# Kernel optimization log

Measured on AMD Instinct MI355X. Metric: run time of the kernel, lower is better.

Reference implementation:

```python
import jax, jax.numpy as jnp
from jax import lax
import numpy as np

HID = 150     # FFNN hidden dim
EMB = 300     # GloVe dim (input_dim)
LSTM = 200    # lstm_dim -> state_dim = 400
T = 768       # tokens in doc
VOCAB = 50000


def _ffnn(x, W1, b1, W2, b2, W3, b3):
    h = jax.nn.relu(x @ W1.T + b1)
    h = jax.nn.relu(h @ W2.T + b2)
    return h @ W3.T + b3


def _lstm_dir(x, Wih, Whh, b):
    H = Whh.shape[1]
    def step(carry, xt):
        h, c = carry
        z = xt @ Wih.T + h @ Whh.T + b
        i, f, g, o = jnp.split(z, 4, axis=-1)
        c = jax.nn.sigmoid(f) * c + jax.nn.sigmoid(i) * jnp.tanh(g)
        h = jax.nn.sigmoid(o) * jnp.tanh(c)
        return (h, c), h
    init = (jnp.zeros((H,), x.dtype), jnp.zeros((H,), x.dtype))
    _, hs = lax.scan(step, init, x)
    return hs


def setup_inputs():
    key = jax.random.key(0)
    ks = iter(jax.random.split(key, 40))
    def w(shape, s=0.05):
        return jax.random.normal(next(ks), shape, jnp.float32) * s
    state = 2 * LSTM
    span = 2 * state + EMB + 1   # 1101
    pair = 3 * span              # 3303
    z = lambda n: jnp.zeros((n,), jnp.float32)
    return {
        'tokens': jax.random.randint(next(ks), (T,), 0, VOCAB),
        'emb': w((VOCAB, EMB), 0.3),
        'Wih_f': w((4 * LSTM, EMB)), 'Whh_f': w((4 * LSTM, LSTM)), 'b_f': z(4 * LSTM),
        'Wih_b': w((4 * LSTM, EMB)), 'Whh_b': w((4 * LSTM, LSTM)), 'b_b': z(4 * LSTM),
        'aW1': w((HID, state)), 'ab1': z(HID), 'aW2': w((HID, HID)), 'ab2': z(HID), 'aW3': w((1, HID)), 'ab3': z(1),
        'sW1': w((HID, span)), 'sb1': z(HID), 'sW2': w((HID, HID)), 'sb2': z(HID), 'sW3': w((1, HID)), 'sb3': z(1),
        'pW1': w((HID, pair)), 'pb1': z(HID), 'pW2': w((HID, HID)), 'pb2': z(HID), 'pW3': w((1, HID)), 'pb3': z(1),
    }


def reference(tokens, emb, Wih_f, Whh_f, b_f, Wih_b, Whh_b, b_b,
              aW1, ab1, aW2, ab2, aW3, ab3,
              sW1, sb1, sW2, sb2, sW3, sb3,
              pW1, pb1, pW2, pb2, pW3, pb3):
    Tn = tokens.shape[0]
    x = emb[tokens]  # (T, 300) frozen GloVe embeds
    h = jnp.concatenate([_lstm_dir(x, Wih_f, Whh_f, b_f),
                         _lstm_dir(x[::-1], Wih_b, Whh_b, b_b)[::-1]], axis=-1)  # (T, 400)
    # dropout omitted (eval mode / identity)
    attn_logits = _ffnn(h, aW1, ab1, aW2, ab2, aW3, ab3)[:, 0]  # per-token attn score (T,)
    gs, i1s, i2s = [], [], []
    for n in range(1, 11):  # span widths 1..10
        starts = jnp.arange(Tn - n + 1)
        idx = starts[:, None] + jnp.arange(n)[None, :]           # (S_n, n)
        wgt = jax.nn.softmax(attn_logits[idx], axis=-1)          # per-span softmax over LSTM-state scores
        pooled = jnp.einsum('sn,snd->sd', wgt, x[idx])           # attention pools raw embeds (as original)
        g = jnp.concatenate([h[starts], h[starts + n - 1], pooled,
                             jnp.full((Tn - n + 1, 1), float(n), jnp.float32)], axis=-1)
        gs.append(g); i1s.append(starts); i2s.append(starts + n - 1)
    g = jnp.concatenate(gs, 0)                                    # (S, 1101)
    i1 = jnp.concatenate(i1s, 0); i2 = jnp.concatenate(i2s, 0)
    S = g.shape[0]
    sm = _ffnn(g, sW1, sb1, sW2, sb2, sW3, sb3)[:, 0]             # span scores (S,)
    order = jnp.argsort(-sm)                                      # stable desc sort, as Python sorted(reverse=True)
    i1o, i2o = i1[order], i2[order]
    # greedy overlap filter: keep span if fully taken OR both endpoints free; mark taken only when kept
    def body(k, carry):
        taken, keep = carry
        a, b = i1o[k], i2o[k]
        offs = jnp.clip(a + jnp.arange(10), 0, Tn - 1)
        valid = (a + jnp.arange(10)) <= b
        all_taken = jnp.all(jnp.where(valid, taken[offs], True))
        ok = all_taken | (~taken[a] & ~taken[b])
        keep = keep.at[k].set(ok)
        taken = taken.at[offs].max(valid & ok)
        return (taken, keep)
    _, keep = lax.fori_loop(0, S, body, (jnp.zeros((Tn,), bool), jnp.zeros((S,), bool)))
    K = int(round(Tn * 0.4))
    rank = jnp.cumsum(keep.astype(jnp.int32))
    pos = jnp.where(keep & (rank <= K), rank - 1, S)
    sel = jnp.argsort(pos)[:K]            # first K kept spans, score order (>=T width-1 spans always kept)
    sel = sel[jnp.argsort(i1o[sel])]      # stable sort by span start
    g_f = g[order][sel]; sm_f = sm[order][sel]
    i1_f = i1o[sel]; i2_f = i2o[sel]
    ii, jj = np.tril_indices(K, -1)       # row-major == nested (i, j<i) loop order
    pairs = jnp.concatenate([g_f[ii], g_f[jj], g_f[ii] * g_f[jj]], axis=-1)  # (P, 3303)
    sa = _ffnn(pairs, pW1, pb1, pW2, pb2, pW3, pb3)[:, 0]
    # sij[i, j] = sm_i + sm_j + sa_ij for j < i; diag/upper = 0 (the epsilon antecedent)
    sij = jnp.zeros((K, K), jnp.float32).at[ii, jj].set(sm_f[ii] + sm_f[jj] + sa)
    return sij, i1_f, i2_f
```

## Files before the change

kernel.cpp:

```cpp
#include <hip/hip_runtime.h>
#include <hip/hip_bf16.h>
#include <math.h>
#include <float.h>

#define TN      768
#define EMBD    300
#define XPAD    304
#define LSTMD   200
#define G4      800
#define STATE   400
#define HIDD    150
#define NPADC   160
#define SPAND   1101
#define KP      1120
#define NSPANS  7635
#define NSEL    307
#define SORTN   8192

typedef unsigned long long ull;
typedef __attribute__((ext_vector_type(8))) short bf16x8;
typedef __attribute__((ext_vector_type(4))) float mf32x4;

#define OFF_X       0u
#define OFF_ZXF     233472u
#define OFF_ZXB     847872u
#define OFF_H       1462272u
#define OFF_ATTN    1769472u
#define OFF_I1      1770496u
#define OFF_I2      1778176u
#define OFF_SM      1785856u
#define OFF_SELK    1793536u
#define OFF_SELSPAN 1794048u
#define OFF_SMF     1794560u
#define OFF_A       1795072u
#define OFF_B       1844224u
#define OFF_WTF     1893376u
#define OFF_WTB     2133376u
#define OFF_AW1T    2373376u
#define OFF_AW2T    2437376u
#define OFF_SW1T    2461376u
#define OFF_SW2T    2640576u
#define OFF_PW1AT   2664576u
#define OFF_PW1BT   2843776u
#define OFF_PW1CT   3022976u
#define OFF_PW2T    3202176u
#define OFF_G       3226176u
#define OFF_PW1CB   11777376u
#define OFF_PW2B    11866976u

#define REP50(M) M(0) M(1) M(2) M(3) M(4) M(5) M(6) M(7) M(8) M(9) \
 M(10) M(11) M(12) M(13) M(14) M(15) M(16) M(17) M(18) M(19) \
 M(20) M(21) M(22) M(23) M(24) M(25) M(26) M(27) M(28) M(29) \
 M(30) M(31) M(32) M(33) M(34) M(35) M(36) M(37) M(38) M(39) \
 M(40) M(41) M(42) M(43) M(44) M(45) M(46) M(47) M(48) M(49)

__device__ __forceinline__ float sigf(float x) { return 1.f / (1.f + __expf(-x)); }
__device__ __forceinline__ float tanhf_(float x) {
    x = fminf(15.f, fmaxf(-15.f, x));
    float e = __expf(2.f * x);
    return (e - 1.f) / (e + 1.f);
}
__device__ __forceinline__ unsigned short f2bf(float v) {
    __hip_bfloat16 h = __float2bfloat16(v);
    return *(unsigned short*)&h;
}

__global__ void k_gather(const int* __restrict__ tokens, const float* __restrict__ emb,
                         float* __restrict__ x) {
    int t = blockIdx.x;
    int tok = tokens[t];
    for (int d = threadIdx.x; d < XPAD; d += 256)
        x[t * XPAD + d] = (d < EMBD) ? emb[(size_t)tok * EMBD + d] : 0.f;
}

__global__ void k_transpose(const float* __restrict__ src, float* __restrict__ dst,
                            int N, int K, int srcStride, int colOff, int Npad) {
    int k = blockIdx.x;
    int n = blockIdx.y * 256 + threadIdx.x;
    if (n >= Npad) return;
    float v = 0.f;
    if (k < K && n < N) v = src[(size_t)n * srcStride + colOff + k];
    dst[(size_t)k * Npad + n] = v;
}

__global__ void k_bf16w(const float* __restrict__ pW1, const float* __restrict__ pW2,
                        unsigned short* __restrict__ pw1cb,
                        unsigned short* __restrict__ pw2b) {
    int r = blockIdx.x;
    for (int k = threadIdx.x; k < 1120; k += 256) {
        float v = (r < 150 && k < 1101) ? pW1[(size_t)r * 3303 + 2202 + k] : 0.f;
        pw1cb[(size_t)r * 1120 + k] = f2bf(v);
    }
    for (int k = threadIdx.x; k < 160; k += 256) {
        float v = (r < 150 && k < 150) ? pW2[(size_t)r * 150 + k] : 0.f;
        pw2b[(size_t)r * 160 + k] = f2bf(v);
    }
}

__global__ void k_zx(const float* __restrict__ x, const float* __restrict__ WTf,
                     const float* __restrict__ WTb, const float* __restrict__ bf,
                     const float* __restrict__ bb, float* __restrict__ zxf,
                     float* __restrict__ zxb) {
    __shared__ float xl[8 * XPAD];
    int tid = threadIdx.x;
    int bm = blockIdx.x, dir = blockIdx.y;
    for (int l = tid; l < 8 * XPAD; l += 256) xl[l] = x[(size_t)(bm * 8) * XPAD + l];
    __syncthreads();
    const float* WT = dir ? WTb : WTf;
    const float* bv = dir ? bb : bf;
    float* zx = dir ? zxb : zxf;
    for (int jj = 0; jj < 4; ++jj) {
        int n = tid + 256 * jj;
        if (n >= G4) break;
        float acc[8] = {0, 0, 0, 0, 0, 0, 0, 0};
        for (int k = 0; k < EMBD; ++k) {
            float wv = WT[(size_t)k * G4 + n];
#pragma unroll
            for (int r = 0; r < 8; ++r) acc[r] = fmaf(xl[r * XPAD + k], wv, acc[r]);
        }
        float bias = bv[n];
#pragma unroll
        for (int r = 0; r < 8; ++r) {
            int row = bm * 8 + r;
            int trow = dir ? (TN - 1 - row) : row;
            zx[(size_t)trow * G4 + n] = acc[r] + bias;
        }
    }
}

__global__ __launch_bounds__(256, 1) void k_lstm_mb8(const float* __restrict__ zxf,
                                                     const float* __restrict__ zxb,
                                                     const float* __restrict__ Whh_f,
                                                     const float* __restrict__ Whh_b,
                                                     float* __restrict__ hcat,
                                                     ull* __restrict__ hqL2,
                                                     ull* __restrict__ hqL3) {
    int blk = blockIdx.x;
    int lane8 = blk & 7;
    if (lane8 >= 2) return;
    int dir = lane8, b = blk >> 3;
    int tid = threadIdx.x;

    const float* zx = dir ? zxb : zxf;
    const float* Whh = dir ? Whh_b : Whh_f;
    ull* hq2d = hqL2 + (size_t)dir * TN * 256;
    ull* hq3d = hqL3 + (size_t)dir * TN * 256;
    __shared__ __align__(16) float hprev[LSTMD];
    __shared__ float zl[200];
    bool active = tid < 200;
    int q = tid / 50, u = tid % 50;
    int gr_row = q * 200 + b * 50 + u;
    int grs = active ? gr_row : 0;
    const float4* wr = (const float4*)(Whh + (size_t)grs * LSTMD);
#define WDECL(i) float4 w##i = wr[i];
    REP50(WDECL)
#undef WDECL
    float c = 0.f;
    for (int l = tid; l < LSTMD; l += 256) hprev[l] = 0.f;
    int remote_idx = (tid < b * 50) ? tid : tid + 50;
    int use_fast = 4;
    __syncthreads();
    float zpre = zx[grs];
    for (int t = 0; t < TN; ++t) {
        float acc = zpre;
        const float4* h4 = (const float4*)hprev;
#define WFMA(i) { float4 hv = h4[i]; \
        acc = fmaf(w##i.x, hv.x, acc); acc = fmaf(w##i.y, hv.y, acc); \
        acc = fmaf(w##i.z, hv.z, acc); acc = fmaf(w##i.w, hv.w, acc); }
        REP50(WFMA)
#undef WFMA
        if (active) zl[tid] = acc;
        __syncthreads();
        int trow = dir ? (TN - 1 - t) : t;
        if (tid < 50) {
            float zi = zl[tid], zf = zl[50 + tid], zg = zl[100 + tid], zo = zl[150 + tid];
            c = sigf(zf) * c + sigf(zi) * tanhf_(zg);
            float h = sigf(zo) * tanhf_(c);
            hcat[(size_t)trow * STATE + dir * LSTMD + b * 50 + tid] = h;
            hprev[b * 50 + tid] = h;
            if (t + 1 < TN) {
                ull pk = (ull)__float_as_uint(h) | ((ull)(unsigned)(t + 1) << 32);
                size_t slot = (size_t)t * 256 + b * 50 + tid;
                (void)__hip_atomic_exchange(&hq2d[slot], pk, __ATOMIC_RELAXED,
                                            __HIP_MEMORY_SCOPE_WORKGROUP);
                __hip_atomic_store(&hq3d[slot], pk, __ATOMIC_RELAXED,
                                   __HIP_MEMORY_SCOPE_AGENT);
            }
        }
        if (t + 1 < TN) {
            zpre = zx[(size_t)(t + 1) * G4 + grs];
            if (tid < 150) {
                size_t slot = (size_t)t * 256 + remote_idx;
                ull v = 0;
                bool got = false;
                if (use_fast > 0) {
                    for (int it = 0; it < 8; ++it) {
                        ull probe = ~0ull;
                        __hip_atomic_compare_exchange_strong(
                            &hq2d[slot], &probe, ~0ull, __ATOMIC_RELAXED,
                            __ATOMIC_RELAXED, __HIP_MEMORY_SCOPE_WORKGROUP);
                        if ((unsigned)(probe >> 32) == (unsigned)(t + 1)) {
                            v = probe; got = true; break;
                        }
                    }
                    use_fast = got ? 4 : (use_fast - 1);
                }
                if (!got) {
                    do {
                        v = __hip_atomic_load(&hq3d[slot], __ATOMIC_RELAXED,
                                              __HIP_MEMORY_SCOPE_AGENT);
                    } while ((unsigned)(v >> 32) != (unsigned)(t + 1));
                }
                hprev[remote_idx] = __uint_as_float((unsigned)v);
            }
            __syncthreads();
        }
    }
}

__global__ void k_attn(const float* __restrict__ hcat, const float* __restrict__ aW1T,
                       const float* __restrict__ ab1, const float* __restrict__ aW2T,
                       const float* __restrict__ ab2, const float* __restrict__ aW3,
                       const float* __restrict__ ab3, float* __restrict__ attn) {
    __shared__ float hrow[STATE];
    __shared__ float l1[NPADC];
    __shared__ float l2[NPADC];
    __shared__ float red[256];
    int t = blockIdx.x, tid = threadIdx.x;
    for (int d = tid; d < STATE; d += 256) hrow[d] = hcat[(size_t)t * STATE + d];
    __syncthreads();
    if (tid < HIDD) {
        float acc = ab1[tid];
        for (int k = 0; k < STATE; ++k) acc = fmaf(hrow[k], aW1T[(size_t)k * NPADC + tid], acc);
        l1[tid] = fmaxf(acc, 0.f);
    }
    __syncthreads();
    if (tid < HIDD) {
        float acc = ab2[tid];
        for (int k = 0; k < HIDD; ++k) acc = fmaf(l1[k], aW2T[(size_t)k * NPADC + tid], acc);
        l2[tid] = fmaxf(acc, 0.f);
    }
    __syncthreads();
    float partial = (tid < HIDD) ? l2[tid] * aW3[tid] : 0.f;
    red[tid] = partial;
    __syncthreads();
    for (int s = 128; s > 0; s >>= 1) {
        if (tid < s) red[tid] += red[tid + s];
        __syncthreads();
    }
    if (tid == 0) attn[t] = red[0] + ab3[0];
}

__global__ void k_spans(const float* __restrict__ attn, const float* __restrict__ hcat,
                        const float* __restrict__ x, float* __restrict__ g,
                        int* __restrict__ i1s, int* __restrict__ i2s) {
    int s = blockIdx.x;
    int n = 1, base = 0;
    while (s >= base + (TN - n + 1)) { base += TN - n + 1; n++; }
    int a = s - base, b = a + n - 1;
    int lane = threadIdx.x;
    float e[10];
    float mx = -FLT_MAX;
#pragma unroll
    for (int k = 0; k < 10; ++k)
        if (k < n) { e[k] = attn[a + k]; mx = fmaxf(mx, e[k]); }
    float ssum = 0.f;
#pragma unroll
    for (int k = 0; k < 10; ++k)
        if (k < n) { e[k] = __expf(e[k] - mx); ssum += e[k]; }
    float w[10];
#pragma unroll
    for (int k = 0; k < 10; ++k) w[k] = (k < n) ? e[k] / ssum : 0.f;

    float* grow = g + (size_t)s * KP;
    for (int d = lane; d < STATE; d += 64) grow[d] = hcat[(size_t)a * STATE + d];
    for (int d = lane; d < STATE; d += 64) grow[STATE + d] = hcat[(size_t)b * STATE + d];
    for (int d = lane; d < EMBD; d += 64) {
        float p = 0.f;
#pragma unroll
        for (int k = 0; k < 10; ++k)
            if (k < n) p = fmaf(w[k], x[(size_t)(a + k) * XPAD + d], p);
        grow[2 * STATE + d] = p;
    }
    if (lane == 0) { grow[1100] = (float)n; i1s[s] = a; i2s[s] = b; }
    for (int d = SPAND + lane; d < KP; d += 64) grow[d] = 0.f;
}

__global__ void k_sm(const float* __restrict__ g, const float* __restrict__ sW1T,
                     const float* __restrict__ sb1, const float* __restrict__ sW2T,
                     const float* __restrict__ sb2, const float* __restrict__ sW3,
                     const float* __restrict__ sb3, float* __restrict__ smo) {
    __shared__ float As[32 * 33];
    __shared__ float Bs[32 * NPADC];
    __shared__ float L1[32 * 161];
    int tid = threadIdx.x;
    int tx = tid & 31, ty = tid >> 5;
    int row0 = blockIdx.x * 32;
    float acc[4][5] = {};
    for (int kb = 0; kb < KP; kb += 32) {
        for (int l = tid; l < 32 * 32; l += 256) {
            int r = l >> 5, cc = l & 31;
            int gr = row0 + r;
            As[r * 33 + cc] = (gr < NSPANS) ? g[(size_t)gr * KP + kb + cc] : 0.f;
        }
        for (int l = tid; l < 32 * NPADC; l += 256) {
            int r = l / NPADC, cc = l - NPADC * r;
            Bs[l] = sW1T[(size_t)(kb + r) * NPADC + cc];
        }
        __syncthreads();
        for (int kk = 0; kk < 32; ++kk) {
            float bv[5];
#pragma unroll
            for (int jn = 0; jn < 5; ++jn) bv[jn] = Bs[kk * NPADC + tx + 32 * jn];
#pragma unroll
            for (int i4 = 0; i4 < 4; ++i4) {
                float av = As[(ty * 4 + i4) * 33 + kk];
#pragma unroll
                for (int jn = 0; jn < 5; ++jn) acc[i4][jn] = fmaf(av, bv[jn], acc[i4][jn]);
            }
        }
        __syncthreads();
    }
#pragma unroll
    for (int i4 = 0; i4 < 4; ++i4)
#pragma unroll
        for (int jn = 0; jn < 5; ++jn) {
            int nn = tx + 32 * jn;
            float v = acc[i4][jn] + (nn < HIDD ? sb1[nn] : 0.f);
            L1[(ty * 4 + i4) * 161 + nn] = fmaxf(v, 0.f);
        }
    __syncthreads();
    float acc2[4][5] = {};
    for (int kk = 0; kk < HIDD; ++kk) {
        float bv[5];
#pragma unroll
        for (int jn = 0; jn < 5; ++jn) bv[jn] = sW2T[(size_t)kk * NPADC + tx + 32 * jn];
#pragma unroll
        for (int i4 = 0; i4 < 4; ++i4) {
            float av = L1[(ty * 4 + i4) * 161 + kk];
#pragma unroll
            for (int jn = 0; jn < 5; ++jn) acc2[i4][jn] = fmaf(av, bv[jn], acc2[i4][jn]);
        }
    }
    float part[4];
#pragma unroll
    for (int i4 = 0; i4 < 4; ++i4) {
        float p = 0.f;
#pragma unroll
        for (int jn = 0; jn < 5; ++jn) {
            int nn = tx + 32 * jn;
            float v = acc2[i4][jn] + (nn < HIDD ? sb2[nn] : 0.f);
            v = fmaxf(v, 0.f);
            p = fmaf(v, (nn < HIDD ? sW3[nn] : 0.f), p);
        }
        part[i4] = p;
    }
    for (int s = 16; s > 0; s >>= 1)
#pragma unroll
        for (int i4 = 0; i4 < 4; ++i4) part[i4] += __shfl_xor(part[i4], s, 32);
    if (tx == 0)
#pragma unroll
        for (int i4 = 0; i4 < 4; ++i4) {
            int gr = row0 + ty * 4 + i4;
            if (gr < NSPANS) smo[gr] = part[i4] + sb3[0];
        }
}

__global__ __launch_bounds__(1024) void k_sortsel(const float* __restrict__ sm,
                                                  const int* __restrict__ i1s,
                                                  const int* __restrict__ i2s,
                                                  int* __restrict__ selk,
                                                  int* __restrict__ selspan,
                                                  float* __restrict__ smf,
                                                  float* __restrict__ out) {
    __shared__ float ks[SORTN];
    __shared__ unsigned short id16[SORTN];
    __shared__ int ka2[512];
    __shared__ int va2[512];
    int tid = threadIdx.x;
    for (int i = tid; i < SORTN; i += 1024) {
        ks[i] = (i < NSPANS) ? sm[i] : -FLT_MAX;
        id16[i] = (unsigned short)i;
    }
    __syncthreads();
    for (int size = 2; size <= SORTN; size <<= 1) {
        for (int stride = size >> 1; stride > 0; stride >>= 1) {
            for (int t = tid; t < SORTN / 2; t += 1024) {
                int i = ((t & ~(stride - 1)) << 1) | (t & (stride - 1));
                int j = i + stride;
                float ki = ks[i], kj = ks[j];
                unsigned short ai = id16[i], aj = id16[j];
                bool less_ji = (kj > ki) || (kj == ki && aj < ai);
                bool asc = ((i & size) == 0);
                if (less_ji == asc) {
                    ks[i] = kj; ks[j] = ki;
                    id16[i] = aj; id16[j] = ai;
                }
            }
            __syncthreads();
        }
    }
    unsigned* abu = reinterpret_cast<unsigned*>(ks);
    for (int k = tid; k < NSPANS; k += 1024) {
        int sid = id16[k];
        abu[k] = (unsigned)i1s[sid] | ((unsigned)i2s[sid] << 16);
    }
    __syncthreads();
    if (tid < 64) {
        int l = tid;
        unsigned tk = 0;
        int cnt = 0;
        for (int k = 0; k < NSPANS && cnt < NSEL; ++k) {
            unsigned ab = abu[k];
            int a = (int)(ab & 0xFFFFu), b = (int)(ab >> 16);
            int lo = a - (l << 5), hi = b - (l << 5);
            lo = lo < 0 ? 0 : lo;
            hi = hi > 31 ? 31 : hi;
            unsigned m = 0;
            if (hi >= lo) {
                unsigned upper = (hi == 31) ? 0xFFFFFFFFu : ((1u << (hi + 1)) - 1u);
                m = upper & ~((1u << lo) - 1u);
            }
            bool cov = ((tk & m) == m);
            bool all_taken = __all((int)cov);
            int la = a >> 5, lb = b >> 5;
            unsigned long long bal_a = __ballot((int)((l == la) && ((tk >> (a & 31)) & 1u)));
            unsigned long long bal_b = __ballot((int)((l == lb) && ((tk >> (b & 31)) & 1u)));
            bool ok = all_taken || (bal_a == 0ull && bal_b == 0ull);
            if (ok) {
                tk |= m;
                if (l == 0) selk[cnt] = k;
                cnt++;
            }
        }
    }
    __syncthreads();
    if (tid < 512) {
        int r = tid;
        int key = 0x7FFFFFFF;
        if (r < NSEL) {
            int k = selk[r];
            int a = (int)(abu[k] & 0xFFFFu);
            key = (a << 9) | r;
        }
        ka2[r] = key;
        va2[r] = r;
    }
    __syncthreads();
    for (int size = 2; size <= 512; size <<= 1) {
        for (int stride = size >> 1; stride > 0; stride >>= 1) {
            if (tid < 256) {
                int t = tid;
                int i = ((t & ~(stride - 1)) << 1) | (t & (stride - 1));
                int j = i + stride;
                int ki = ka2[i], kj = ka2[j];
                bool asc = ((i & size) == 0);
                if ((kj < ki) == asc) {
                    ka2[i] = kj; ka2[j] = ki;
                    int vi = va2[i]; va2[i] = va2[j]; va2[j] = vi;
                }
            }
            __syncthreads();
        }
    }
    if (tid < NSEL) {
        int r = va2[tid];
        int k = selk[r];
        int sid = id16[k];
        unsigned ab = abu[k];
        selspan[tid] = sid;
        smf[tid] = sm[sid];
        out[NSEL * NSEL + tid] = (float)(ab & 0xFFFFu);
        out[NSEL * NSEL + NSEL + tid] = (float)(ab >> 16);
    }
}

__global__ void k_AB(const float* __restrict__ g, const int* __restrict__ selspan,
                     const float* __restrict__ pW1aT, const float* __restrict__ pW1bT,
                     const float* __restrict__ pb1, float* __restrict__ Aw,
                     float* __restrict__ Bw) {
    __shared__ float grow[KP];
    int r = blockIdx.x, which = blockIdx.y;
    int sid = selspan[r];
    int tid = threadIdx.x;
    for (int d = tid; d < KP; d += 256) grow[d] = g[(size_t)sid * KP + d];
    __syncthreads();
    if (tid < NPADC) {
        const float* WT = which ? pW1bT : pW1aT;
        float acc = 0.f;
        for (int k = 0; k < KP; ++k) acc = fmaf(grow[k], WT[(size_t)k * NPADC + tid], acc);
        if (which == 0) acc += (tid < HIDD ? pb1[tid] : 0.f);
        (which ? Bw : Aw)[(size_t)r * NPADC + tid] = acc;
    }
}

__global__ __launch_bounds__(256, 1) void k_pairs_mfma(
    const float* __restrict__ g, const int* __restrict__ selspan,
    const float* __restrict__ smf, const float* __restrict__ Aw,
    const float* __restrict__ Bw, const unsigned short* __restrict__ pw1cb,
    const unsigned short* __restrict__ pw2b, const float* __restrict__ pb2,
    const float* __restrict__ pW3, const float* __restrict__ pb3,
    float* __restrict__ out) {
    int i = blockIdx.x;
    int j0 = blockIdx.y * 32;
    if (j0 >= i) return;
    __shared__ __align__(16) unsigned short Abuf[32][232];
    __shared__ __align__(16) unsigned short Btb[160][232];
    __shared__ __align__(16) unsigned short L1b[32][168];
    __shared__ float BwS[32][160];
    __shared__ float AwS[160];
    __shared__ float GiS[224];
    __shared__ float pb2S[160], pw3S[160];
    __shared__ float parts[4][32];
    int tid = threadIdx.x;
    int lane = tid & 63, wv = tid >> 6;
    int l15 = lane & 15, lg = lane >> 4;
    int sidi = selspan[i];

    if (tid < 160) {
        AwS[tid] = Aw[(size_t)i * NPADC + tid];
        pb2S[tid] = (tid < HIDD) ? pb2[tid] : 0.f;
        pw3S[tid] = (tid < HIDD) ? pW3[tid] : 0.f;
    }
    for (int idx = tid; idx < 32 * 160; idx += 256) {
        int r = idx / 160; int c = idx - r * 160;
        int j = j0 + r;
        BwS[r][c] = Bw[(size_t)(j < i ? j : 0) * NPADC + c];
    }
    mf32x4 acc[2][3];
#pragma unroll
    for (int m = 0; m < 2; ++m)
#pragma unroll
        for (int t = 0; t < 3; ++t) acc[m][t] = (mf32x4){0.f, 0.f, 0.f, 0.f};

    for (int kc = 0; kc < KP; kc += 224) {
        if (tid < 56)
            *(float4*)&GiS[tid * 4] = *(const float4*)&g[(size_t)sidi * KP + kc + tid * 4];
        for (int idx = tid; idx < 160 * 28; idx += 256) {
            int r = idx / 28, s = idx - r * 28;
            uint4 v = *(const uint4*)(pw1cb + (size_t)r * 1120 + kc + s * 8);
            *(uint4*)&Btb[r][s * 8] = v;
        }
        __syncthreads();
        for (int idx = tid; idx < 32 * 56; idx += 256) {
            int r = idx / 56, s = idx - r * 56;
            int j = j0 + r;
            float4 gj = {0.f, 0.f, 0.f, 0.f};
            if (j < i) gj = *(const float4*)&g[(size_t)selspan[j] * KP + kc + s * 4];
            float4 gi = *(const float4*)&GiS[s * 4];
            ushort4 u;
            u.x = f2bf(gj.x * gi.x); u.y = f2bf(gj.y * gi.y);
            u.z = f2bf(gj.z * gi.z); u.w = f2bf(gj.w * gi.w);
            *(ushort4*)&Abuf[r][s * 4] = u;
        }
        __syncthreads();
#pragma unroll
        for (int kk = 0; kk < 7; ++kk) {
            int ko = kk * 32 + lg * 8;
            bf16x8 a0 = *(const bf16x8*)&Abuf[l15][ko];
            bf16x8 a1 = *(const bf16x8*)&Abuf[16 + l15][ko];
#pragma unroll
            for (int t = 0; t < 3; ++t) {
                int n = wv + 4 * t;
                if (n < 10) {
                    bf16x8 bb = *(const bf16x8*)&Btb[n * 16 + l15][ko];
                    acc[0][t] = __builtin_amdgcn_mfma_f32_16x16x32_bf16(a0, bb, acc[0][t], 0, 0, 0);
                    acc[1][t] = __builtin_amdgcn_mfma_f32_16x16x32_bf16(a1, bb, acc[1][t], 0, 0, 0);
                }
            }
        }
        __syncthreads();
    }
#pragma unroll
    for (int m = 0; m < 2; ++m)
#pragma unroll
        for (int t = 0; t < 3; ++t) {
            int n = wv + 4 * t;
            if (n < 10) {
#pragma unroll
                for (int q = 0; q < 4; ++q) {
                    int row = m * 16 + lg * 4 + q;
                    int col = n * 16 + l15;
                    float v = acc[m][t][q] + AwS[col] + BwS[row][col];
                    L1b[row][col] = f2bf(fmaxf(v, 0.f));
                }
            }
        }
    for (int idx = tid; idx < 160 * 20; idx += 256) {
        int r = idx / 20, s = idx - r * 20;
        *(uint4*)&Btb[r][s * 8] = *(const uint4*)(pw2b + (size_t)r * 160 + s * 8);
    }
    __syncthreads();
    mf32x4 acc2[2][3];
#pragma unroll
    for (int m = 0; m < 2; ++m)
#pragma unroll
        for (int t = 0; t < 3; ++t) acc2[m][t] = (mf32x4){0.f, 0.f, 0.f, 0.f};
#pragma unroll
    for (int kk = 0; kk < 5; ++kk) {
        int ko = kk * 32 + lg * 8;
        bf16x8 a0 = *(const bf16x8*)&L1b[l15][ko];
        bf16x8 a1 = *(const bf16x8*)&L1b[16 + l15][ko];
#pragma unroll
        for (int t = 0; t < 3; ++t) {
            int n = wv + 4 * t;
            if (n < 10) {
                bf16x8 bb = *(const bf16x8*)&Btb[n * 16 + l15][ko];
                acc2[0][t] = __builtin_amdgcn_mfma_f32_16x16x32_bf16(a0, bb, acc2[0][t], 0, 0, 0);
                acc2[1][t] = __builtin_amdgcn_mfma_f32_16x16x32_bf16(a1, bb, acc2[1][t], 0, 0, 0);
            }
        }
    }
    float s[2][4] = {};
#pragma unroll
    for (int m = 0; m < 2; ++m)
#pragma unroll
        for (int t = 0; t < 3; ++t) {
            int n = wv + 4 * t;
            if (n < 10) {
#pragma unroll
                for (int q = 0; q < 4; ++q) {
                    int col = n * 16 + l15;
                    float v = fmaxf(acc2[m][t][q] + pb2S[col], 0.f);
                    s[m][q] = fmaf(v, pw3S[col], s[m][q]);
                }
            }
        }
#pragma unroll
    for (int off = 1; off < 16; off <<= 1)
#pragma unroll
        for (int m = 0; m < 2; ++m)
#pragma unroll
            for (int q = 0; q < 4; ++q) s[m][q] += __shfl_xor(s[m][q], off);
    if (l15 == 0) {
#pragma unroll
        for (int m = 0; m < 2; ++m)
#pragma unroll
            for (int q = 0; q < 4; ++q) parts[wv][m * 16 + lg * 4 + q] = s[m][q];
    }
    __syncthreads();
    if (tid < 32) {
        float sa = parts[0][tid] + parts[1][tid] + parts[2][tid] + parts[3][tid];
        int j = j0 + tid;
        if (j < i) out[(size_t)i * NSEL + j] = smf[i] + smf[j] + sa + pb3[0];
    }
}

extern "C" void kernel_launch(void* const* d_in, const int* in_sizes, int n_in,
                              void* d_out, int out_size, void* d_ws, size_t ws_size,
                              hipStream_t stream) {
    (void)in_sizes; (void)n_in; (void)ws_size;
    const int* tokens  = (const int*)d_in[0];
    const float* emb   = (const float*)d_in[1];
    const float* Wih_f = (const float*)d_in[2];
    const float* Whh_f = (const float*)d_in[3];
    const float* b_f   = (const float*)d_in[4];
    const float* Wih_b = (const float*)d_in[5];
    const float* Whh_b = (const float*)d_in[6];
    const float* b_b   = (const float*)d_in[7];
    const float* aW1 = (const float*)d_in[8];  const float* ab1 = (const float*)d_in[9];
    const float* aW2 = (const float*)d_in[10]; const float* ab2 = (const float*)d_in[11];
    const float* aW3 = (const float*)d_in[12]; const float* ab3 = (const float*)d_in[13];
    const float* sW1 = (const float*)d_in[14]; const float* sb1 = (const float*)d_in[15];
    const float* sW2 = (const float*)d_in[16]; const float* sb2 = (const float*)d_in[17];
    const float* sW3 = (const float*)d_in[18]; const float* sb3 = (const float*)d_in[19];
    const float* pW1 = (const float*)d_in[20]; const float* pb1 = (const float*)d_in[21];
    const float* pW2 = (const float*)d_in[22]; const float* pb2 = (const float*)d_in[23];
    const float* pW3 = (const float*)d_in[24]; const float* pb3 = (const float*)d_in[25];
    float* W = (float*)d_ws;
    float* out = (float*)d_out;
    ull* hqL2 = (ull*)(W + OFF_G);
    ull* hqL3 = hqL2 + (size_t)2 * TN * 256;
    unsigned short* pw1cb = (unsigned short*)(W + OFF_PW1CB);
    unsigned short* pw2b  = (unsigned short*)(W + OFF_PW2B);

    hipMemsetAsync(d_out, 0, (size_t)out_size * sizeof(float), stream);
    hipMemsetAsync(hqL2, 0, (size_t)4 * TN * 256 * sizeof(ull), stream);

    k_gather<<<TN, 256, 0, stream>>>(tokens, emb, W + OFF_X);

    k_transpose<<<dim3(300, 4), 256, 0, stream>>>(Wih_f, W + OFF_WTF, 800, 300, 300, 0, 800);
    k_transpose<<<dim3(300, 4), 256, 0, stream>>>(Wih_b, W + OFF_WTB, 800, 300, 300, 0, 800);
    k_transpose<<<dim3(400, 1), 256, 0, stream>>>(aW1, W + OFF_AW1T, 150, 400, 400, 0, NPADC);
    k_transpose<<<dim3(150, 1), 256, 0, stream>>>(aW2, W + OFF_AW2T, 150, 150, 150, 0, NPADC);
    k_transpose<<<dim3(KP, 1), 256, 0, stream>>>(sW1, W + OFF_SW1T, 150, SPAND, SPAND, 0, NPADC);
    k_transpose<<<dim3(150, 1), 256, 0, stream>>>(sW2, W + OFF_SW2T, 150, 150, 150, 0, NPADC);
    k_transpose<<<dim3(KP, 1), 256, 0, stream>>>(pW1, W + OFF_PW1AT, 150, SPAND, 3303, 0, NPADC);
    k_transpose<<<dim3(KP, 1), 256, 0, stream>>>(pW1, W + OFF_PW1BT, 150, SPAND, 3303, 1101, NPADC);
    k_bf16w<<<160, 256, 0, stream>>>(pW1, pW2, pw1cb, pw2b);

    k_zx<<<dim3(96, 2), 256, 0, stream>>>(W + OFF_X, W + OFF_WTF, W + OFF_WTB, b_f, b_b,
                                          W + OFF_ZXF, W + OFF_ZXB);
    k_lstm_mb8<<<32, 256, 0, stream>>>(W + OFF_ZXF, W + OFF_ZXB, Whh_f, Whh_b, W + OFF_H,
                                       hqL2, hqL3);
    k_attn<<<TN, 256, 0, stream>>>(W + OFF_H, W + OFF_AW1T, ab1, W + OFF_AW2T, ab2, aW3, ab3,
                                   W + OFF_ATTN);
    k_spans<<<NSPANS, 64, 0, stream>>>(W + OFF_ATTN, W + OFF_H, W + OFF_X, W + OFF_G,
                                       (int*)(W + OFF_I1), (int*)(W + OFF_I2));
    k_sm<<<(NSPANS + 31) / 32, 256, 0, stream>>>(W + OFF_G, W + OFF_SW1T, sb1, W + OFF_SW2T, sb2,
                                                 sW3, sb3, W + OFF_SM);
    k_sortsel<<<1, 1024, 0, stream>>>(W + OFF_SM, (int*)(W + OFF_I1), (int*)(W + OFF_I2),
                                      (int*)(W + OFF_SELK), (int*)(W + OFF_SELSPAN),
                                      W + OFF_SMF, out);
    k_AB<<<dim3(NSEL, 2), 256, 0, stream>>>(W + OFF_G, (int*)(W + OFF_SELSPAN), W + OFF_PW1AT,
                                            W + OFF_PW1BT, pb1, W + OFF_A, W + OFF_B);
    k_pairs_mfma<<<dim3(NSEL, 10), 256, 0, stream>>>(W + OFF_G, (int*)(W + OFF_SELSPAN),
                                                     W + OFF_SMF, W + OFF_A, W + OFF_B,
                                                     pw1cb, pw2b, pb2, pW3, pb3, out);
}
```

Before: 2.218 ms.

## Fold weight prep into LSTM kernel blocks and merge gather/transpose launches

Merges the embedding gather and both Wih transposes into one launch. The remaining weight transposes and bf16 conversions move into extra blocks of the LSTM kernel, so they run alongside the serial recurrence instead of as separate launches. The LSTM dot product is also split across four accumulators to shorten the dependent FMA chain. This cuts kernel launch count and hides prep work behind the latency-bound LSTM, at the risk of the extra blocks competing with LSTM blocks for CUs or memory bandwidth. The four-way split also changes the floating-point summation order slightly.

```diff
diff --git a/kernel.cpp b/kernel.cpp
--- a/kernel.cpp
+++ b/kernel.cpp
@@ -42,8 +42,6 @@
 #define OFF_SW2T    2640576u
 #define OFF_PW1AT   2664576u
 #define OFF_PW1BT   2843776u
-#define OFF_PW1CT   3022976u
-#define OFF_PW2T    3202176u
 #define OFF_G       3226176u
 #define OFF_PW1CB   11777376u
 #define OFF_PW2B    11866976u
@@ -65,35 +63,23 @@
     return *(unsigned short*)&h;
 }
 
-__global__ void k_gather(const int* __restrict__ tokens, const float* __restrict__ emb,
-                         float* __restrict__ x) {
-    int t = blockIdx.x;
-    int tok = tokens[t];
-    for (int d = threadIdx.x; d < XPAD; d += 256)
-        x[t * XPAD + d] = (d < EMBD) ? emb[(size_t)tok * EMBD + d] : 0.f;
-}
-
-__global__ void k_transpose(const float* __restrict__ src, float* __restrict__ dst,
-                            int N, int K, int srcStride, int colOff, int Npad) {
-    int k = blockIdx.x;
-    int n = blockIdx.y * 256 + threadIdx.x;
-    if (n >= Npad) return;
-    float v = 0.f;
-    if (k < K && n < N) v = src[(size_t)n * srcStride + colOff + k];
-    dst[(size_t)k * Npad + n] = v;
-}
-
-__global__ void k_bf16w(const float* __restrict__ pW1, const float* __restrict__ pW2,
-                        unsigned short* __restrict__ pw1cb,
-                        unsigned short* __restrict__ pw2b) {
-    int r = blockIdx.x;
-    for (int k = threadIdx.x; k < 1120; k += 256) {
-        float v = (r < 150 && k < 1101) ? pW1[(size_t)r * 3303 + 2202 + k] : 0.f;
-        pw1cb[(size_t)r * 1120 + k] = f2bf(v);
-    }
-    for (int k = threadIdx.x; k < 160; k += 256) {
-        float v = (r < 150 && k < 150) ? pW2[(size_t)r * 150 + k] : 0.f;
-        pw2b[(size_t)r * 160 + k] = f2bf(v);
+__global__ void k_pre0(const int* __restrict__ tokens, const float* __restrict__ emb,
+                       float* __restrict__ x, const float* __restrict__ Wih_f,
+                       const float* __restrict__ Wih_b, float* __restrict__ wtf,
+                       float* __restrict__ wtb) {
+    int b = blockIdx.x, tid = threadIdx.x;
+    if (b < TN) {
+        int tok = tokens[b];
+        for (int d = tid; d < XPAD; d += 256)
+            x[b * XPAD + d] = (d < EMBD) ? emb[(size_t)tok * EMBD + d] : 0.f;
+    } else if (b < TN + 1200) {
+        int bb = b - TN;
+        int k = bb >> 2, n = ((bb & 3) << 8) + tid;
+        if (n < G4) wtf[(size_t)k * G4 + n] = Wih_f[(size_t)n * EMBD + k];
+    } else {
+        int bb = b - TN - 1200;
+        int k = bb >> 2, n = ((bb & 3) << 8) + tid;
+        if (n < G4) wtb[(size_t)k * G4 + n] = Wih_b[(size_t)n * EMBD + k];
     }
 }
 
@@ -128,18 +114,54 @@
     }
 }
 
-__global__ __launch_bounds__(256, 1) void k_lstm_mb8(const float* __restrict__ zxf,
-                                                     const float* __restrict__ zxb,
-                                                     const float* __restrict__ Whh_f,
-                                                     const float* __restrict__ Whh_b,
-                                                     float* __restrict__ hcat,
-                                                     ull* __restrict__ hqL2,
-                                                     ull* __restrict__ hqL3) {
+__device__ void prep_tr(const float* __restrict__ src, float* __restrict__ dst,
+                        int N, int K, int stride, int off, int Npad, int totalK,
+                        int part, int nparts, int tid) {
+    int total = totalK * Npad;
+    for (int idx = part * 256 + tid; idx < total; idx += nparts * 256) {
+        int k = idx / Npad, n = idx - k * Npad;
+        dst[idx] = (k < K && n < N) ? src[(size_t)n * stride + off + k] : 0.f;
+    }
+}
+__device__ void prep_bf(const float* __restrict__ src, unsigned short* __restrict__ dst,
+                        int R, int C, int stride, int off, int NR, int NC,
+                        int part, int nparts, int tid) {
+    int total = NR * NC;
+    for (int idx = part * 256 + tid; idx < total; idx += nparts * 256) {
+        int r = idx / NC, c = idx - r * NC;
+        float v = (r < R && c < C) ? src[(size_t)r * stride + off + c] : 0.f;
+        dst[idx] = f2bf(v);
+    }
+}
+
+__global__ __launch_bounds__(256, 1) void k_lstm_mb8(
+    const float* __restrict__ zxf, const float* __restrict__ zxb,
+    const float* __restrict__ Whh_f, const float* __restrict__ Whh_b,
+    float* __restrict__ hcat, ull* __restrict__ hqL2, ull* __restrict__ hqL3,
+    const float* __restrict__ aW1, const float* __restrict__ aW2,
+    const float* __restrict__ sW1, const float* __restrict__ sW2,
+    const float* __restrict__ pW1, const float* __restrict__ pW2,
+    float* __restrict__ aW1T, float* __restrict__ aW2T,
+    float* __restrict__ sW1T, float* __restrict__ sW2T,
+    float* __restrict__ pW1AT, float* __restrict__ pW1BT,
+    unsigned short* __restrict__ pw1cb, unsigned short* __restrict__ pw2b) {
     int blk = blockIdx.x;
+    int tid = threadIdx.x;
+    if (blk >= 32) {
+        int p = blk - 32;
+        if (p < 4)       prep_tr(aW1, aW1T, 150, 400, 400, 0, 160, 400, p, 4, tid);
+        else if (p < 6)  prep_tr(aW2, aW2T, 150, 150, 150, 0, 160, 150, p - 4, 2, tid);
+        else if (p < 18) prep_tr(sW1, sW1T, 150, SPAND, SPAND, 0, 160, KP, p - 6, 12, tid);
+        else if (p < 20) prep_tr(sW2, sW2T, 150, 150, 150, 0, 160, 150, p - 18, 2, tid);
+        else if (p < 32) prep_tr(pW1, pW1AT, 150, SPAND, 3303, 0, 160, KP, p - 20, 12, tid);
+        else if (p < 44) prep_tr(pW1, pW1BT, 150, SPAND, 3303, 1101, 160, KP, p - 32, 12, tid);
+        else if (p < 56) prep_bf(pW1, pw1cb, 150, SPAND, 3303, 2202, 160, KP, p - 44, 12, tid);
+        else             prep_bf(pW2, pw2b, 150, 150, 150, 0, 160, 160, p - 56, 2, tid);
+        return;
+    }
     int lane8 = blk & 7;
     if (lane8 >= 2) return;
     int dir = lane8, b = blk >> 3;
-    int tid = threadIdx.x;
 
     const float* zx = dir ? zxb : zxf;
     const float* Whh = dir ? Whh_b : Whh_f;
@@ -162,14 +184,14 @@
     __syncthreads();
     float zpre = zx[grs];
     for (int t = 0; t < TN; ++t) {
-        float acc = zpre;
+        float a0 = zpre, a1 = 0.f, a2 = 0.f, a3 = 0.f;
         const float4* h4 = (const float4*)hprev;
 #define WFMA(i) { float4 hv = h4[i]; \
-        acc = fmaf(w##i.x, hv.x, acc); acc = fmaf(w##i.y, hv.y, acc); \
-        acc = fmaf(w##i.z, hv.z, acc); acc = fmaf(w##i.w, hv.w, acc); }
+        a0 = fmaf(w##i.x, hv.x, a0); a1 = fmaf(w##i.y, hv.y, a1); \
+        a2 = fmaf(w##i.z, hv.z, a2); a3 = fmaf(w##i.w, hv.w, a3); }
         REP50(WFMA)
 #undef WFMA
-        if (active) zl[tid] = acc;
+        if (active) zl[tid] = (a0 + a1) + (a2 + a3);
         __syncthreads();
         int trow = dir ? (TN - 1 - t) : t;
         if (tid < 50) {
@@ -677,22 +699,14 @@
     hipMemsetAsync(d_out, 0, (size_t)out_size * sizeof(float), stream);
     hipMemsetAsync(hqL2, 0, (size_t)4 * TN * 256 * sizeof(ull), stream);
 
-    k_gather<<<TN, 256, 0, stream>>>(tokens, emb, W + OFF_X);
-
-    k_transpose<<<dim3(300, 4), 256, 0, stream>>>(Wih_f, W + OFF_WTF, 800, 300, 300, 0, 800);
-    k_transpose<<<dim3(300, 4), 256, 0, stream>>>(Wih_b, W + OFF_WTB, 800, 300, 300, 0, 800);
-    k_transpose<<<dim3(400, 1), 256, 0, stream>>>(aW1, W + OFF_AW1T, 150, 400, 400, 0, NPADC);
-    k_transpose<<<dim3(150, 1), 256, 0, stream>>>(aW2, W + OFF_AW2T, 150, 150, 150, 0, NPADC);
-    k_transpose<<<dim3(KP, 1), 256, 0, stream>>>(sW1, W + OFF_SW1T, 150, SPAND, SPAND, 0, NPADC);
-    k_transpose<<<dim3(150, 1), 256, 0, stream>>>(sW2, W + OFF_SW2T, 150, 150, 150, 0, NPADC);
-    k_transpose<<<dim3(KP, 1), 256, 0, stream>>>(pW1, W + OFF_PW1AT, 150, SPAND, 3303, 0, NPADC);
-    k_transpose<<<dim3(KP, 1), 256, 0, stream>>>(pW1, W + OFF_PW1BT, 150, SPAND, 3303, 1101, NPADC);
-    k_bf16w<<<160, 256, 0, stream>>>(pW1, pW2, pw1cb, pw2b);
-
+    k_pre0<<<TN + 2400, 256, 0, stream>>>(tokens, emb, W + OFF_X, Wih_f, Wih_b,
+                                          W + OFF_WTF, W + OFF_WTB);
     k_zx<<<dim3(96, 2), 256, 0, stream>>>(W + OFF_X, W + OFF_WTF, W + OFF_WTB, b_f, b_b,
                                           W + OFF_ZXF, W + OFF_ZXB);
-    k_lstm_mb8<<<32, 256, 0, stream>>>(W + OFF_ZXF, W + OFF_ZXB, Whh_f, Whh_b, W + OFF_H,
-                                       hqL2, hqL3);
+    k_lstm_mb8<<<90, 256, 0, stream>>>(W + OFF_ZXF, W + OFF_ZXB, Whh_f, Whh_b, W + OFF_H,
+                                       hqL2, hqL3, aW1, aW2, sW1, sW2, pW1, pW2,
+                                       W + OFF_AW1T, W + OFF_AW2T, W + OFF_SW1T, W + OFF_SW2T,
+                                       W + OFF_PW1AT, W + OFF_PW1BT, pw1cb, pw2b);
     k_attn<<<TN, 256, 0, stream>>>(W + OFF_H, W + OFF_AW1T, ab1, W + OFF_AW2T, ab2, aW3, ab3,
                                    W + OFF_ATTN);
     k_spans<<<NSPANS, 64, 0, stream>>>(W + OFF_ATTN, W + OFF_H, W + OFF_X, W + OFF_G,
```

Result: slower. 2.993 ms (+34.9%).
